# Performance work log

Hardware: AMD Instinct MI355X
Metric: run time of the kernel (lower is better)

## Reference

```python
import jax, jax.numpy as jnp
import numpy as np

B, S, D = 4, 2048, 2048


def setup_inputs() -> dict:
    key = jax.random.key(0)
    ks = jax.random.split(key, 9)
    scale = 1.0 / np.sqrt(D)
    x = jax.random.normal(ks[0], (B, S, D), dtype=jnp.float32)
    # causal mask, broadcast to [B, S, S]; 0 -> masked
    mask = jnp.broadcast_to(jnp.tril(jnp.ones((S, S), dtype=jnp.int32)), (B, S, S))
    Wq = jax.random.normal(ks[1], (D, D), dtype=jnp.float32) * scale
    Wk = jax.random.normal(ks[2], (D, D), dtype=jnp.float32) * scale
    Wv = jax.random.normal(ks[3], (D, D), dtype=jnp.float32) * scale
    Wp = jax.random.normal(ks[4], (D, D), dtype=jnp.float32) * scale
    bq = jnp.zeros((D,), jnp.float32)
    bk = jnp.zeros((D,), jnp.float32)
    bv = jnp.zeros((D,), jnp.float32)
    bp = jnp.zeros((D,), jnp.float32)
    return {"x": x, "mask": mask, "Wq": Wq, "bq": bq, "Wk": Wk, "bk": bk,
            "Wv": Wv, "bv": bv, "Wp": Wp, "bp": bp}


def reference(x, mask, Wq, bq, Wk, bk, Wv, bv, Wp, bp):
    # single-head scaled dot-product attention (cache=None path, eval mode)
    d_k = x.shape[-1]
    inv_std = 1.0 / jnp.sqrt(jnp.asarray(d_k, x.dtype))
    q = jnp.einsum('bsd,ed->bse', x, Wq) + bq  # nn.Linear: x @ W^T + b
    k = jnp.einsum('bsd,ed->bse', x, Wk) + bk
    v = jnp.einsum('bsd,ed->bse', x, Wv) + bv
    scores = jnp.einsum('bqd,bkd->bqk', q, k) * inv_std  # [B,S,S]
    scores = jnp.where(mask == 0, jnp.asarray(-jnp.inf, scores.dtype), scores)
    attn = jax.nn.softmax(scores, axis=-1)
    ctx = jnp.einsum('bqk,bkd->bqd', attn, v)
    out = jnp.einsum('bsd,ed->bse', ctx, Wp) + bp
    return out
```

## Files before the change

kernel.cpp:

```cpp
#include <hip/hip_runtime.h>
#include <hip/hip_bf16.h>
#include <type_traits>
#include <math.h>


typedef __bf16 bf16x8_t __attribute__((ext_vector_type(8)));
typedef float f32x4_t __attribute__((ext_vector_type(4)));
typedef unsigned short u16x8_t __attribute__((ext_vector_type(8)));

__device__ inline unsigned short f2bf(float f) {
  unsigned int u = __builtin_bit_cast(unsigned int, f);
  unsigned int r = u + 0x7fffu + ((u >> 16) & 1u);
  return (unsigned short)(r >> 16);
}

__device__ inline void gl2lds16(const unsigned short* g, unsigned short* l) {
  __builtin_amdgcn_global_load_lds(
      (const __attribute__((address_space(1))) unsigned int*)g,
      (__attribute__((address_space(3))) unsigned int*)l, 16, 0, 0);
}

__device__ __forceinline__ bf16x8_t ldf(const unsigned short* p) {
  return __builtin_bit_cast(bf16x8_t, *(const u16x8_t*)p);
}

#define MF(a_, b_, c_) \
  (c_) = __builtin_amdgcn_mfma_f32_16x16x32_bf16((a_), (b_), (c_), 0, 0, 0)
#define FENCE() asm volatile("" ::: "memory")
#define BAR() __builtin_amdgcn_s_barrier()
#define LGK0() asm volatile("s_waitcnt lgkmcnt(0)" ::: "memory")
#define VM6() asm volatile("s_waitcnt vmcnt(6)" ::: "memory")
#define SCHED0() __builtin_amdgcn_sched_barrier(0)
#define PRIO(x) __builtin_amdgcn_s_setprio(x)

__global__ __launch_bounds__(256) void cast_f32_bf16(
    const float* __restrict__ in, unsigned short* __restrict__ out, long n4) {
  long i = blockIdx.x * 256L + threadIdx.x;
  if (i >= n4) return;
  float4 f = ((const float4*)in)[i];
  ushort4 u;
  u.x = f2bf(f.x); u.y = f2bf(f.y); u.z = f2bf(f.z); u.w = f2bf(f.w);
  ((ushort4*)out)[i] = u;
}

__global__ __launch_bounds__(256) void cast_w4(
    const float* __restrict__ w0, const float* __restrict__ w1,
    const float* __restrict__ w2, const float* __restrict__ w3,
    unsigned short* __restrict__ o0, unsigned short* __restrict__ o1,
    unsigned short* __restrict__ o2, unsigned short* __restrict__ o3,
    long n4) {
  long i = blockIdx.x * 256L + threadIdx.x;
  if (i >= n4) return;
  const float* in; unsigned short* out;
  switch (blockIdx.y) {
    case 0: in = w0; out = o0; break;
    case 1: in = w1; out = o1; break;
    case 2: in = w2; out = o2; break;
    default: in = w3; out = o3; break;
  }
  float4 f = ((const float4*)in)[i];
  ushort4 u;
  u.x = f2bf(f.x); u.y = f2bf(f.y); u.z = f2bf(f.z); u.w = f2bf(f.w);
  ((ushort4*)out)[i] = u;
}

__device__ __forceinline__ void g256_kloop(
    const unsigned short* __restrict__ A, const unsigned short* __restrict__ B,
    int K, int Keff, unsigned short* smem, f32x4_t (&acc)[8][4]) {
  const int tid = threadIdx.x;
  const int lane = tid & 63;
  const int wave = tid >> 6;
  const int wr = wave >> 2;
  const int wc = wave & 3;
  const int fr = lane & 15;
  const int q4 = lane >> 4;
  const int s0 = (q4 ^ (fr & 7)) * 8;
  const int s1 = ((q4 + 4) ^ (fr & 7)) * 8;
  const size_t rowK =
      (size_t)(wave * 8 + (lane >> 3)) * (size_t)K +
      (size_t)(((lane & 7) ^ ((lane >> 3) & 7)) * 8);
  const size_t K64 = (size_t)64 * K;
  const size_t K128 = (size_t)128 * K;
  const int wofs = wave * 512;
  const int NT = Keff >> 6;

#define STG(gp_, lh_)                        \
  do {                                       \
    const unsigned short* g_ = (gp_) + rowK; \
    gl2lds16(g_, (lh_) + wofs);              \
    gl2lds16(g_ + K64, (lh_) + 4096 + wofs); \
  } while (0)

  STG(A, smem);
  STG(A + K128, smem + 8192);
  STG(B, smem + 16384);
  STG(B + K128, smem + 24576);
  STG(B + 64, smem + 32768 + 16384);
  STG(B + K128 + 64, smem + 32768 + 24576);
  STG(A + 64, smem + 32768);
  VM6();
  FENCE();
  BAR();

  for (int kt = 0; kt < NT; ++kt) {
    unsigned short* bc = smem + ((kt & 1) << 15);
    unsigned short* nb = smem + (((kt + 1) & 1) << 15);
    const unsigned short* Ahc = bc + wr * 8192 + fr * 64;
    const unsigned short* Bhc =
        bc + 16384 + (wc >> 1) * 8192 + (wc & 1) * 4096 + fr * 64;
    int k1 = (kt + 1) << 6; if (k1 >= Keff) k1 -= Keff;
    int k2 = (kt + 2) << 6; if (k2 >= Keff) k2 -= Keff;

    bf16x8_t bfr[4][2], af01[2][2], af25[4][2], af67[2][2];

#pragma unroll
    for (int n = 0; n < 4; ++n) {
      const unsigned short* p = Bhc + n * 1024;
      bfr[n][0] = ldf(p + s0);
      bfr[n][1] = ldf(p + s1);
    }
#pragma unroll
    for (int m = 0; m < 2; ++m) {
      const unsigned short* p = Ahc + m * 1024;
      af01[m][0] = ldf(p + s0);
      af01[m][1] = ldf(p + s1);
    }
    STG(A + K128 + k1, nb + 8192);
    FENCE(); BAR(); LGK0(); SCHED0();
    PRIO(1);
#pragma unroll
    for (int m = 0; m < 2; ++m)
#pragma unroll
      for (int n = 0; n < 4; ++n) {
        MF(af01[m][0], bfr[n][0], acc[m][n]);
        MF(af01[m][1], bfr[n][1], acc[m][n]);
      }
    PRIO(0);
    FENCE(); BAR();

#pragma unroll
    for (int m = 0; m < 4; ++m) {
      const unsigned short* p = Ahc + (m + 2) * 1024;
      af25[m][0] = ldf(p + s0);
      af25[m][1] = ldf(p + s1);
    }
    STG(B + k2, bc + 16384);
    FENCE(); BAR(); LGK0(); SCHED0();
    PRIO(1);
#pragma unroll
    for (int m = 0; m < 2; ++m)
#pragma unroll
      for (int n = 0; n < 4; ++n) {
        MF(af25[m][0], bfr[n][0], acc[2 + m][n]);
        MF(af25[m][1], bfr[n][1], acc[2 + m][n]);
      }
    PRIO(0);
    FENCE(); BAR();

#pragma unroll
    for (int m = 0; m < 2; ++m) {
      const unsigned short* p = Ahc + (m + 6) * 1024;
      af67[m][0] = ldf(p + s0);
      af67[m][1] = ldf(p + s1);
    }
    STG(B + K128 + k2, bc + 24576);
    FENCE(); BAR(); LGK0(); SCHED0();
    PRIO(1);
#pragma unroll
    for (int m = 0; m < 2; ++m)
#pragma unroll
      for (int n = 0; n < 4; ++n) {
        MF(af25[2 + m][0], bfr[n][0], acc[4 + m][n]);
        MF(af25[2 + m][1], bfr[n][1], acc[4 + m][n]);
      }
    PRIO(0);
    FENCE(); BAR();

    STG(A + k2, bc);
    FENCE(); BAR(); LGK0(); SCHED0();
    PRIO(1);
#pragma unroll
    for (int m = 0; m < 2; ++m)
#pragma unroll
      for (int n = 0; n < 4; ++n) {
        MF(af67[m][0], bfr[n][0], acc[6 + m][n]);
        MF(af67[m][1], bfr[n][1], acc[6 + m][n]);
      }
    PRIO(0);
    VM6();
    FENCE(); BAR();
  }
#undef STG
}

template <int MODE, typename OutT>
__global__ __launch_bounds__(512, 2) void gemm256_nt(
    const unsigned short* __restrict__ A, const unsigned short* __restrict__ B,
    OutT* __restrict__ C, const float* __restrict__ bias, float alpha,
    int N, int K, size_t sA, size_t sB, size_t sC) {
  int lin = blockIdx.y * gridDim.x + blockIdx.x;
  const int nwg = gridDim.x * gridDim.y;
  lin = (lin & 7) * (nwg >> 3) + (lin >> 3);
  const int bm = (lin / gridDim.x) * 256;
  const int bn = (lin % gridDim.x) * 256;
  if (MODE == 1 && bn >= bm + 256) return;
  int Keff = K;
  if (MODE == 2) { int kl = bm + 256; Keff = kl < K ? kl : K; }

  A += (size_t)blockIdx.z * sA + (size_t)bm * K;
  B += (size_t)blockIdx.z * sB + (size_t)bn * K;
  C += (size_t)blockIdx.z * sC;

  __shared__ unsigned short smem[65536];
  f32x4_t acc[8][4] = {};
  g256_kloop(A, B, K, Keff, smem, acc);

  const int tid = threadIdx.x;
  const int lane = tid & 63;
  const int wave = tid >> 6;
  const int wr = wave >> 2, wc = wave & 3;
  const int fr = lane & 15, q4 = lane >> 4;
  const int r0 = bm + wr * 128 + q4 * 4;
  const int c0 = bn + wc * 64 + fr;
#pragma unroll
  for (int n = 0; n < 4; ++n) {
    const int col = c0 + n * 16;
    const float bs = bias ? bias[col] : 0.f;
#pragma unroll
    for (int m = 0; m < 8; ++m) {
      const int row = r0 + m * 16;
#pragma unroll
      for (int r = 0; r < 4; ++r) {
        float v = acc[m][n][r] * alpha + bs;
        if constexpr (std::is_same_v<OutT, float>)
          C[(size_t)(row + r) * N + col] = v;
        else
          C[(size_t)(row + r) * N + col] = f2bf(v);
      }
    }
  }
}

__global__ __launch_bounds__(512, 2) void gemm256_qkv(
    const unsigned short* __restrict__ A, const unsigned short* __restrict__ Bw,
    unsigned short* __restrict__ Q, unsigned short* __restrict__ Kd,
    unsigned short* __restrict__ Vt,
    const float* __restrict__ bq, const float* __restrict__ bk,
    const float* __restrict__ bv, int K, int D, int S) {
  int lin = blockIdx.y * gridDim.x + blockIdx.x;
  const int nwg = gridDim.x * gridDim.y;
  lin = (lin & 7) * (nwg >> 3) + (lin >> 3);
  const int bm = (lin / gridDim.x) * 256;
  const int bn = (lin % gridDim.x) * 256;

  __shared__ unsigned short smem[65536];
  f32x4_t acc[8][4] = {};
  g256_kloop(A + (size_t)bm * K, Bw + (size_t)bn * K, K, K, smem, acc);

  const int tid = threadIdx.x;
  const int lane = tid & 63;
  const int wave = tid >> 6;
  const int wr = wave >> 2, wc = wave & 3;
  const int fr = lane & 15, q4 = lane >> 4;
  const int r0 = bm + wr * 128 + q4 * 4;
  const int c0 = bn + wc * 64 + fr;
#pragma unroll
  for (int n = 0; n < 4; ++n) {
    const int col = c0 + n * 16;
    const int sel = col >> 11;
    const int idx = col & (D - 1);
    const float bs = (sel == 0 ? bq : sel == 1 ? bk : bv)[idx];
#pragma unroll
    for (int m = 0; m < 8; ++m) {
      const int row = r0 + m * 16;
      if (sel < 2) {
        unsigned short* dst = sel == 0 ? Q : Kd;
#pragma unroll
        for (int r = 0; r < 4; ++r)
          dst[(size_t)(row + r) * D + idx] = f2bf(acc[m][n][r] + bs);
      } else {
        const int b = row >> 11;
        const int s = row & (S - 1);
        ushort4 pack;
        pack.x = f2bf(acc[m][n][0] + bs);
        pack.y = f2bf(acc[m][n][1] + bs);
        pack.z = f2bf(acc[m][n][2] + bs);
        pack.w = f2bf(acc[m][n][3] + bs);
        *(ushort4*)&Vt[(size_t)b * D * S + (size_t)idx * S + s] = pack;
      }
    }
  }
}

__global__ __launch_bounds__(256) void softmax_causal(
    const float* __restrict__ Sc, unsigned short* __restrict__ P, int n) {
  const int row = blockIdx.x;
  const int q = row & (n - 1);
  const float* srow = Sc + (size_t)row * n;
  unsigned short* prow = P + (size_t)row * n;
  const int tid = threadIdx.x, lane = tid & 63, wid = tid >> 6;
  __shared__ float red[4];

  float m = -3.0e38f;
  for (int j = tid; j <= q; j += 256) m = fmaxf(m, srow[j]);
#pragma unroll
  for (int o = 32; o; o >>= 1) m = fmaxf(m, __shfl_down(m, o, 64));
  if (lane == 0) red[wid] = m;
  __syncthreads();
  m = fmaxf(fmaxf(red[0], red[1]), fmaxf(red[2], red[3]));
  __syncthreads();

  float s = 0.f;
  for (int j = tid; j <= q; j += 256) s += __expf(srow[j] - m);
#pragma unroll
  for (int o = 32; o; o >>= 1) s += __shfl_down(s, o, 64);
  if (lane == 0) red[wid] = s;
  __syncthreads();
  s = red[0] + red[1] + red[2] + red[3];
  const float inv = 1.f / s;

  for (int j = tid; j < n; j += 256) {
    float v = (j <= q) ? __expf(srow[j] - m) * inv : 0.f;
    prow[j] = f2bf(v);
  }
}

extern "C" void kernel_launch(void* const* d_in, const int* in_sizes, int n_in,
                              void* d_out, int out_size, void* d_ws, size_t ws_size,
                              hipStream_t stream) {
  const int B = 4, S = 2048, D = 2048;
  const int M = B * S;

  const float* x  = (const float*)d_in[0];
  const float* Wq = (const float*)d_in[2];
  const float* bq = (const float*)d_in[3];
  const float* Wk = (const float*)d_in[4];
  const float* bk = (const float*)d_in[5];
  const float* Wv = (const float*)d_in[6];
  const float* bv = (const float*)d_in[7];
  const float* Wp = (const float*)d_in[8];
  const float* bp = (const float*)d_in[9];
  float* out = (float*)d_out;

  char* ws = (char*)d_ws;
  const size_t MB = 1ull << 20;
  unsigned short* xb   = (unsigned short*)(ws + 0);
  unsigned short* wqkv = (unsigned short*)(ws + 32 * MB);
  unsigned short* wpb  = (unsigned short*)(ws + 56 * MB);
  unsigned short* qb   = (unsigned short*)(ws + 64 * MB);
  unsigned short* kb   = (unsigned short*)(ws + 96 * MB);
  unsigned short* vtb  = (unsigned short*)(ws + 160 * MB);
  float*          sc   = (float*)(ws + 192 * MB);
  unsigned short* pb   = qb;
  unsigned short* cb   = kb;

  const long nx = (long)M * D;
  const long nw = (long)D * D;

  cast_f32_bf16<<<dim3((unsigned)((nx / 4 + 255) / 256)), 256, 0, stream>>>(x, xb, nx / 4);
  cast_w4<<<dim3((unsigned)((nw / 4 + 255) / 256), 4), 256, 0, stream>>>(
      Wq, Wk, Wv, Wp,
      wqkv, wqkv + (size_t)D * D, wqkv + 2 * (size_t)D * D, wpb, nw / 4);

  const dim3 blk(512);

  gemm256_qkv<<<dim3(3 * D / 256, M / 256), blk, 0, stream>>>(
      xb, wqkv, qb, kb, vtb, bq, bk, bv, D, D, S);

  const float inv_std = 1.f / sqrtf((float)D);
  gemm256_nt<1, float><<<dim3(S / 256, S / 256, B), blk, 0, stream>>>(
      qb, kb, sc, nullptr, inv_std, S, D, (size_t)S * D, (size_t)S * D, (size_t)S * S);

  softmax_causal<<<dim3(B * S), dim3(256), 0, stream>>>(sc, pb, S);

  gemm256_nt<2, unsigned short><<<dim3(D / 256, S / 256, B), blk, 0, stream>>>(
      pb, vtb, cb, nullptr, 1.f, D, S, (size_t)S * S, (size_t)D * S, (size_t)S * D);

  gemm256_nt<0, float><<<dim3(D / 256, M / 256), blk, 0, stream>>>(
      cb, wpb, out, bp, 1.f, D, D, 0, 0, 0);
}
```

Before: 621.2 us.

## Software-pipeline LDS fragment reads one phase ahead of MFMA in GEMM main loop

After: 599.0 us. 3.6% less time.

```diff
diff --git a/kernel.cpp b/kernel.cpp
--- a/kernel.cpp
+++ b/kernel.cpp
@@ -27,10 +27,15 @@
 #define MF(a_, b_, c_) \
   (c_) = __builtin_amdgcn_mfma_f32_16x16x32_bf16((a_), (b_), (c_), 0, 0, 0)
 #define FENCE() asm volatile("" ::: "memory")
-#define BAR() __builtin_amdgcn_s_barrier()
+#define BARF()              \
+  do {                      \
+    FENCE();                \
+    __builtin_amdgcn_s_barrier(); \
+    FENCE();                \
+  } while (0)
 #define LGK0() asm volatile("s_waitcnt lgkmcnt(0)" ::: "memory")
+#define VM4() asm volatile("s_waitcnt vmcnt(4)" ::: "memory")
 #define VM6() asm volatile("s_waitcnt vmcnt(6)" ::: "memory")
-#define SCHED0() __builtin_amdgcn_sched_barrier(0)
 #define PRIO(x) __builtin_amdgcn_s_setprio(x)
 
 __global__ __launch_bounds__(256) void cast_f32_bf16(
@@ -83,6 +88,8 @@
   const size_t K128 = (size_t)128 * K;
   const int wofs = wave * 512;
   const int NT = Keff >> 6;
+  const int aoff = wr * 8192 + fr * 64;
+  const int boff = 16384 + (wc >> 1) * 8192 + (wc & 1) * 4096 + fr * 64;
 
 #define STG(gp_, lh_)                        \
   do {                                       \
@@ -90,6 +97,22 @@
     gl2lds16(g_, (lh_) + wofs);              \
     gl2lds16(g_ + K64, (lh_) + 4096 + wofs); \
   } while (0)
+
+#define MFMA8(mb_, af_)                          \
+  _Pragma("unroll")                              \
+  for (int n = 0; n < 4; ++n) {                  \
+    MF(af_[0][0], bfr[n][0], acc[(mb_)][n]);     \
+    MF(af_[0][1], bfr[n][1], acc[(mb_)][n]);     \
+    MF(af_[1][0], bfr[n][0], acc[(mb_) + 1][n]); \
+    MF(af_[1][1], bfr[n][1], acc[(mb_) + 1][n]); \
+  }
+
+#define RDA(dst_, base_, mo_)                          \
+  _Pragma("unroll")                                    \
+  for (int m = 0; m < 2; ++m) {                        \
+    dst_[m][0] = ldf((base_) + (m + (mo_)) * 1024 + s0); \
+    dst_[m][1] = ldf((base_) + (m + (mo_)) * 1024 + s1); \
+  }
 
   STG(A, smem);
   STG(A + K128, smem + 8192);
@@ -99,98 +122,74 @@
   STG(B + K128 + 64, smem + 32768 + 24576);
   STG(A + 64, smem + 32768);
   VM6();
-  FENCE();
-  BAR();
+  BARF();
+
+  bf16x8_t bfr[4][2], a01[2][2], a23[2][2], a45[2][2], a67[2][2];
+  {
+    const unsigned short* Bh = smem + boff;
+    const unsigned short* Ah = smem + aoff;
+#pragma unroll
+    for (int n = 0; n < 4; ++n) {
+      bfr[n][0] = ldf(Bh + n * 1024 + s0);
+      bfr[n][1] = ldf(Bh + n * 1024 + s1);
+    }
+    RDA(a01, Ah, 0);
+  }
 
   for (int kt = 0; kt < NT; ++kt) {
     unsigned short* bc = smem + ((kt & 1) << 15);
     unsigned short* nb = smem + (((kt + 1) & 1) << 15);
-    const unsigned short* Ahc = bc + wr * 8192 + fr * 64;
-    const unsigned short* Bhc =
-        bc + 16384 + (wc >> 1) * 8192 + (wc & 1) * 4096 + fr * 64;
+    const unsigned short* Ahc = bc + aoff;
+    const unsigned short* Ahn = nb + aoff;
+    const unsigned short* Bhn = nb + boff;
     int k1 = (kt + 1) << 6; if (k1 >= Keff) k1 -= Keff;
     int k2 = (kt + 2) << 6; if (k2 >= Keff) k2 -= Keff;
 
-    bf16x8_t bfr[4][2], af01[2][2], af25[4][2], af67[2][2];
-
+    RDA(a23, Ahc, 2);
+    STG(A + K128 + k1, nb + 8192);
+    BARF();
+    PRIO(1);
+    MFMA8(0, a01);
+    PRIO(0);
+    BARF();
+
+    RDA(a45, Ahc, 4);
+    STG(B + k2, bc + 16384);
+    BARF();
+    PRIO(1);
+    MFMA8(2, a23);
+    PRIO(0);
+    BARF();
+
+    RDA(a67, Ahc, 6);
+    STG(B + K128 + k2, bc + 24576);
+    BARF();
+    PRIO(1);
+    MFMA8(4, a45);
+    PRIO(0);
+    BARF();
+
+    VM4();
+    LGK0();
+    BARF();
+    STG(A + k2, bc);
+    PRIO(1);
 #pragma unroll
     for (int n = 0; n < 4; ++n) {
-      const unsigned short* p = Bhc + n * 1024;
-      bfr[n][0] = ldf(p + s0);
-      bfr[n][1] = ldf(p + s1);
+      MF(a67[0][0], bfr[n][0], acc[6][n]);
+      MF(a67[0][1], bfr[n][1], acc[6][n]);
+      MF(a67[1][0], bfr[n][0], acc[7][n]);
+      MF(a67[1][1], bfr[n][1], acc[7][n]);
+      bfr[n][0] = ldf(Bhn + n * 1024 + s0);
+      bfr[n][1] = ldf(Bhn + n * 1024 + s1);
     }
-#pragma unroll
-    for (int m = 0; m < 2; ++m) {
-      const unsigned short* p = Ahc + m * 1024;
-      af01[m][0] = ldf(p + s0);
-      af01[m][1] = ldf(p + s1);
-    }
-    STG(A + K128 + k1, nb + 8192);
-    FENCE(); BAR(); LGK0(); SCHED0();
-    PRIO(1);
-#pragma unroll
-    for (int m = 0; m < 2; ++m)
-#pragma unroll
-      for (int n = 0; n < 4; ++n) {
-        MF(af01[m][0], bfr[n][0], acc[m][n]);
-        MF(af01[m][1], bfr[n][1], acc[m][n]);
-      }
+    RDA(a01, Ahn, 0);
     PRIO(0);
-    FENCE(); BAR();
-
-#pragma unroll
-    for (int m = 0; m < 4; ++m) {
-      const unsigned short* p = Ahc + (m + 2) * 1024;
-      af25[m][0] = ldf(p + s0);
-      af25[m][1] = ldf(p + s1);
-    }
-    STG(B + k2, bc + 16384);
-    FENCE(); BAR(); LGK0(); SCHED0();
-    PRIO(1);
-#pragma unroll
-    for (int m = 0; m < 2; ++m)
-#pragma unroll
-      for (int n = 0; n < 4; ++n) {
-        MF(af25[m][0], bfr[n][0], acc[2 + m][n]);
-        MF(af25[m][1], bfr[n][1], acc[2 + m][n]);
-      }
-    PRIO(0);
-    FENCE(); BAR();
-
-#pragma unroll
-    for (int m = 0; m < 2; ++m) {
-      const unsigned short* p = Ahc + (m + 6) * 1024;
-      af67[m][0] = ldf(p + s0);
-      af67[m][1] = ldf(p + s1);
-    }
-    STG(B + K128 + k2, bc + 24576);
-    FENCE(); BAR(); LGK0(); SCHED0();
-    PRIO(1);
-#pragma unroll
-    for (int m = 0; m < 2; ++m)
-#pragma unroll
-      for (int n = 0; n < 4; ++n) {
-        MF(af25[2 + m][0], bfr[n][0], acc[4 + m][n]);
-        MF(af25[2 + m][1], bfr[n][1], acc[4 + m][n]);
-      }
-    PRIO(0);
-    FENCE(); BAR();
-
-    STG(A + k2, bc);
-    FENCE(); BAR(); LGK0(); SCHED0();
-    PRIO(1);
-#pragma unroll
-    for (int m = 0; m < 2; ++m)
-#pragma unroll
-      for (int n = 0; n < 4; ++n) {
-        MF(af67[m][0], bfr[n][0], acc[6 + m][n]);
-        MF(af67[m][1], bfr[n][1], acc[6 + m][n]);
-      }
-    PRIO(0);
-    VM6();
-    FENCE(); BAR();
+    BARF();
   }
 #undef STG
+#undef MFMA8
+#undef RDA
 }
 
 template <int MODE, typename OutT>
```
